# Kernel optimization log

Hardware: AMD Instinct MI355X
Metric: run time of the kernel (lower is better)

Reference implementation:

```python
import jax, jax.numpy as jnp
import numpy as np

GRID = 0.5
NG = 48
NC = 16  # output channels
CHUNK = 256  # atoms per scan step (bounds peak memory)
E2 = float(np.exp(2.0))
# order matches pro_keys ['O','C','N','S'] with vdw_dic
VDW = jnp.array([1.52, 1.7, 1.55, 1.8], dtype=jnp.float32)


def setup_inputs() -> dict:
    key = jax.random.key(0)
    k1, k2, k3 = jax.random.split(key, 3)
    N = 2048
    coords = jax.random.uniform(k1, (N, 3), dtype=jnp.float32) * (NG * GRID)  # [0, 24)
    ch_idx = jax.random.randint(k2, (N,), 0, 4, dtype=jnp.int32)
    fg = jax.random.randint(k3, (N,), 0, 16, dtype=jnp.int32)
    return {"coords": coords, "ch_idx": ch_idx, "fg": fg}


def _channel_weights(ch_idx, fg):
    # base element channel 0..3
    w = jax.nn.one_hot(ch_idx, NC, dtype=jnp.float32)
    # fg routing: 14 -> +ch4 +ch5; 15 -> +ch6 +ch9; 12/13 -> nothing; else -> +ch(fg+4)
    c1 = jnp.where(fg == 14, 4, jnp.where(fg == 15, 6, fg + 4))
    c1 = jnp.where((fg == 12) | (fg == 13), -1, c1)  # one_hot(-1) == zeros
    c2 = jnp.where(fg == 14, 5, jnp.where(fg == 15, 9, -1))
    return w + jax.nn.one_hot(c1, NC, dtype=jnp.float32) + jax.nn.one_hot(c2, NC, dtype=jnp.float32)


def _grid_forward(coords, r, w):
    # coords [N,3], r [N] vdw radii, w [N,16] channel weights -> [16,48,48,48]
    gx = GRID * jnp.arange(NG, dtype=jnp.float32)  # grid point coordinates
    nchunk = coords.shape[0] // CHUNK
    coords_c = coords.reshape(nchunk, CHUNK, 3)
    r_c = r.reshape(nchunk, CHUNK)
    w_c = w.reshape(nchunk, CHUNK, NC)

    def body(acc, args):
        c, rr, ww = args  # [CHUNK,3], [CHUNK], [CHUNK,16]
        dx2 = (c[:, 0, None] - gx) ** 2  # [CHUNK,48]
        dy2 = (c[:, 1, None] - gx) ** 2
        dz2 = (c[:, 2, None] - gx) ** 2
        d2 = dx2[:, :, None, None] + dy2[:, None, :, None] + dz2[:, None, None, :]  # [CHUNK,48,48,48]
        d = jnp.sqrt(d2)
        r_ = rr[:, None, None, None]
        r2 = r_ * r_
        f1 = jnp.exp(-2.0 * d2 / r2)
        f2 = 4.0 * d2 / (E2 * r2) - 12.0 * d / (E2 * r_) + 9.0 / E2
        val = jnp.where(d < r_, f1, jnp.where(d < 1.5 * r_, f2, 0.0))
        acc = acc + jnp.einsum('nc,nxyz->cxyz', ww, val)
        return acc, None

    out, _ = jax.lax.scan(body, jnp.zeros((NC, NG, NG, NG), jnp.float32), (coords_c, r_c, w_c))
    return out


def reference(coords, ch_idx, fg):
    r = VDW[ch_idx]
    w = _channel_weights(ch_idx, fg)
    return _grid_forward(coords, r, w)
```

## Files before the change

### kernel.cpp

```cpp
#include <hip/hip_runtime.h>

#define NG 48
#define NC 16
#define NPTS (NG * NG * NG)
#define E2F 7.3890561f
#define NINE_OVER_E2 1.2180175f
#define LOG2E 1.44269504f

#define BR 4
#define SEGCAP 48
#define SBCAP 512
#define MAXATOMS 2048

__device__ __constant__ float c_vdw[4] = {1.52f, 1.7f, 1.55f, 1.8f};

__device__ __forceinline__ void atom_params(int ci, int f, float r,
                                            float& b0, float& b1, float& b2, int& mask) {
    const float r2 = r * r;
    int c1 = (f == 14) ? 4 : ((f == 15) ? 6 : f + 4);
    if (f == 12 || f == 13) c1 = -1;
    const int c2 = (f == 14) ? 5 : ((f == 15) ? 9 : -1);
    mask = 1 << ci;
    if (c1 >= 0) mask |= 1 << c1;
    if (c2 >= 0) mask |= 1 << c2;
    b0 = -2.0f * LOG2E / r2;
    b1 = 4.0f / (E2F * r2);
    b2 = 12.0f / (E2F * r);
}

__global__ __launch_bounds__(1024)
void build_kernel(const float* __restrict__ coords,
                  const int* __restrict__ ch_idx,
                  const int* __restrict__ fg,
                  float4* __restrict__ segA, float4* __restrict__ segB,
                  int* __restrict__ counts, int natoms)
{
    __shared__ float sx[MAXATOMS], sy[MAXATOMS], sz[MAXATOMS], scut[MAXATOMS];
    __shared__ float sb0[MAXATOMS], sb1[MAXATOMS], sb2[MAXATOMS], sb3[MAXATOMS];
    __shared__ int sCnt[16];

    const int t = threadIdx.x, w = t >> 6, l = t & 63;
    const int n = min(natoms, MAXATOMS);

    for (int i = t; i < n; i += 1024) {
        const float x = coords[3 * i], y = coords[3 * i + 1], z = coords[3 * i + 2];
        const int ci = ch_idx[i], f = fg[i];
        const float r = c_vdw[ci];
        float b0, b1, b2; int mask;
        atom_params(ci, f, r, b0, b1, b2, mask);
        sx[i] = x; sy[i] = y; sz[i] = z; scut[i] = 1.5f * r;
        sb0[i] = b0; sb1[i] = b1; sb2[i] = b2; sb3[i] = __int_as_float(mask);
    }
    __syncthreads();

    const int sb = blockIdx.x;
    const int sbx = sb / 9, sby = (sb / 3) % 3, sbz = sb % 3;
    const float lox = sbx * 8.0f, hix = lox + 7.5f;
    const float loy = sby * 8.0f, hiy = loy + 7.5f;
    const float loz = sbz * 8.0f, hiz = loz + 7.5f;

    int runTot = 0;
    for (int base = 0; base < n; base += 1024) {
        const int a = base + t;
        bool pred = false;
        float ax = 0.f, ay = 0.f, az = 0.f, cut = 0.f;
        if (a < n) {
            ax = sx[a]; ay = sy[a]; az = sz[a]; cut = scut[a];
            const float ddx = fmaxf(fmaxf(lox - ax, ax - hix), 0.f);
            const float ddy = fmaxf(fmaxf(loy - ay, ay - hiy), 0.f);
            const float ddz = fmaxf(fmaxf(loz - az, az - hiz), 0.f);
            pred = fmaf(ddx, ddx, fmaf(ddy, ddy, ddz * ddz)) < cut * cut;
        }
        const unsigned long long m = __ballot(pred);
        if (l == 0) sCnt[w] = __popcll(m);
        __syncthreads();
        int ofs = runTot, tot = 0;
        #pragma unroll
        for (int w2 = 0; w2 < 16; ++w2) {
            const int c = sCnt[w2];
            if (w2 < w) ofs += c;
            tot += c;
        }
        if (pred) {
            const int o = ofs + __popcll(m & ((1ull << l) - 1ull));
            if (o < SBCAP) {
                segA[sb * SBCAP + o] = make_float4(ax, ay, az, cut);
                segB[sb * SBCAP + o] = make_float4(sb0[a], sb1[a], sb2[a], sb3[a]);
            }
        }
        runTot += tot;
        __syncthreads();
    }
    if (t == 0) counts[sb] = min(runTot, SBCAP);
}

__global__ __launch_bounds__(256)
void density_kernel(const float4* __restrict__ segA,
                    const float4* __restrict__ segB,
                    const int* __restrict__ counts,
                    float* __restrict__ out)
{
    __shared__ __align__(16) unsigned char smem[16384];
    __shared__ int sCnt[4];
    float4* const sA = (float4*)smem;
    float4* const sB = sA + 4 * SEGCAP;
    float (*const sRed)[64] = (float (*)[64])smem;

    const int t = threadIdx.x, w = t >> 6, l = t & 63;
    const int bz = blockIdx.x, by = blockIdx.y, bx = blockIdx.z;

    const float blox = bx * 2.0f, bhix = blox + 1.5f;
    const float bloy = by * 2.0f, bhiy = bloy + 1.5f;
    const float bloz = bz * 2.0f, bhiz = bloz + 1.5f;

    const int sb = ((bx >> 2) * 3 + (by >> 2)) * 3 + (bz >> 2);
    const int cnt_sb = counts[sb];
    const float4* const srcA = segA + sb * SBCAP;
    const float4* const srcB = segB + sb * SBCAP;

    const int q = (cnt_sb + 3) >> 2;
    const int i0 = w * q, i1 = min(i0 + q, cnt_sb);
    int myCnt = 0;
    for (int base = i0; base < i1; base += 64) {
        const int idx = base + l;
        bool pred = false;
        float4 pA, pB;
        if (idx < i1) {
            pA = srcA[idx];
            pB = srcB[idx];
            const float ddx = fmaxf(fmaxf(blox - pA.x, pA.x - bhix), 0.f);
            const float ddy = fmaxf(fmaxf(bloy - pA.y, pA.y - bhiy), 0.f);
            const float ddz = fmaxf(fmaxf(bloz - pA.z, pA.z - bhiz), 0.f);
            pred = fmaf(ddx, ddx, fmaf(ddy, ddy, ddz * ddz)) < pA.w * pA.w;
        }
        const unsigned long long m = __ballot(pred);
        if (pred) {
            const int o = myCnt + __popcll(m & ((1ull << l) - 1ull));
            if (o < SEGCAP) { sA[w * SEGCAP + o] = pA; sB[w * SEGCAP + o] = pB; }
        }
        myCnt += __popcll(m);
    }
    if (l == 0) sCnt[w] = min(myCnt, SEGCAP);
    __syncthreads();

    const int c0 = sCnt[0], c1 = sCnt[1], c2 = sCnt[2], c3 = sCnt[3];

    const int tz = l & 3, ty = (l >> 2) & 3, tx = l >> 4;
    const float px = (bx * BR + tx) * 0.5f;
    const float py = (by * BR + ty) * 0.5f;
    const float pz = (bz * BR + tz) * 0.5f;

    float acc[NC];
    #pragma unroll
    for (int c = 0; c < NC; ++c) acc[c] = 0.0f;

    #pragma unroll 1
    for (int s = 0; s < 4; ++s) {
        const int cs = (s == 0) ? c0 : (s == 1) ? c1 : (s == 2) ? c2 : c3;
        const int segbase = s * SEGCAP;
        #pragma unroll 2
        for (int i = w; i < cs; i += 4) {
            const float4 A = sA[segbase + i];
            const float4 B = sB[segbase + i];
            const float dx = px - A.x;
            const float dy = py - A.y;
            const float dz = pz - A.z;
            const float d2 = fmaf(dx, dx, fmaf(dy, dy, dz * dz));
            const float cut2 = A.w * A.w;
            if (d2 < cut2) {
                const float r2 = cut2 * (4.0f / 9.0f);
                const float d  = sqrtf(d2);
                const float f1 = exp2f(B.x * d2);
                const float f2 = fmaf(B.y, d2, fmaf(-B.z, d, NINE_OVER_E2));
                const float val = (d2 < r2) ? f1 : f2;
                const int chan = __builtin_amdgcn_readfirstlane(__float_as_int(B.w));
                #pragma unroll
                for (int c = 0; c < NC; ++c)
                    if (chan & (1 << c)) acc[c] += val;
            }
        }
    }
    __syncthreads();

    #pragma unroll
    for (int c = 0; c < NC; ++c) sRed[w * NC + c][l] = acc[c];
    __syncthreads();

    const int gx = bx * BR + tx, gy = by * BR + ty, gz = bz * BR + tz;
    const int pbase = (gx * NG + gy) * NG + gz;
    #pragma unroll
    for (int k = 0; k < 4; ++k) {
        const int c = w * 4 + k;
        const float s = sRed[0 * NC + c][l] + sRed[1 * NC + c][l] +
                        sRed[2 * NC + c][l] + sRed[3 * NC + c][l];
        out[c * NPTS + pbase] = s;
    }
}

__global__ void prep_kernel(const float* __restrict__ coords,
                            const int* __restrict__ ch_idx,
                            const int* __restrict__ fg,
                            float4* __restrict__ atomA,
                            float4* __restrict__ atomB, int natoms)
{
    const int i = blockIdx.x * blockDim.x + threadIdx.x;
    if (i >= natoms) return;
    const int ci = ch_idx[i], f = fg[i];
    const float r = c_vdw[ci];
    float b0, b1, b2; int mask;
    atom_params(ci, f, r, b0, b1, b2, mask);
    atomA[i] = make_float4(coords[3 * i], coords[3 * i + 1], coords[3 * i + 2], 1.5f * r);
    atomB[i] = make_float4(b0, b1, b2, __int_as_float(mask));
}

__global__ __launch_bounds__(256)
void density_scan_kernel(const float4* __restrict__ atomA,
                         const float4* __restrict__ atomB,
                         float* __restrict__ out, int natoms)
{
    __shared__ __align__(16) unsigned char smem[16384];
    __shared__ int sCnt[4];
    float4* const sA = (float4*)smem;
    float4* const sB = sA + 4 * SEGCAP;
    float (*const sRed)[64] = (float (*)[64])smem;

    const int t = threadIdx.x, w = t >> 6, l = t & 63;
    const int bz = blockIdx.x, by = blockIdx.y, bx = blockIdx.z;

    const float blox = bx * 2.0f, bhix = blox + 1.5f;
    const float bloy = by * 2.0f, bhiy = bloy + 1.5f;
    const float bloz = bz * 2.0f, bhiz = bloz + 1.5f;

    const int quarter = (natoms + 3) >> 2;
    const int a0 = w * quarter, a1 = min(a0 + quarter, natoms);
    int myCnt = 0;
    for (int base = a0; base < a1; base += 64) {
        const int a = base + l;
        bool pred = false; float4 pA;
        if (a < a1) {
            pA = atomA[a];
            const float ddx = fmaxf(fmaxf(blox - pA.x, pA.x - bhix), 0.f);
            const float ddy = fmaxf(fmaxf(bloy - pA.y, pA.y - bhiy), 0.f);
            const float ddz = fmaxf(fmaxf(bloz - pA.z, pA.z - bhiz), 0.f);
            pred = fmaf(ddx, ddx, fmaf(ddy, ddy, ddz * ddz)) < pA.w * pA.w;
        }
        const unsigned long long m = __ballot(pred);
        if (pred) {
            const int o = myCnt + __popcll(m & ((1ull << l) - 1ull));
            if (o < SEGCAP) { sA[w * SEGCAP + o] = pA; sB[w * SEGCAP + o] = atomB[a]; }
        }
        myCnt += __popcll(m);
    }
    if (l == 0) sCnt[w] = min(myCnt, SEGCAP);
    __syncthreads();

    const int c0 = sCnt[0], c1 = sCnt[1], c2 = sCnt[2], c3 = sCnt[3];
    const int tz = l & 3, ty = (l >> 2) & 3, tx = l >> 4;
    const float px = (bx * BR + tx) * 0.5f;
    const float py = (by * BR + ty) * 0.5f;
    const float pz = (bz * BR + tz) * 0.5f;

    float acc[NC];
    #pragma unroll
    for (int c = 0; c < NC; ++c) acc[c] = 0.0f;

    #pragma unroll 1
    for (int s = 0; s < 4; ++s) {
        const int cs = (s == 0) ? c0 : (s == 1) ? c1 : (s == 2) ? c2 : c3;
        const int segbase = s * SEGCAP;
        #pragma unroll 2
        for (int i = w; i < cs; i += 4) {
            const float4 A = sA[segbase + i];
            const float4 B = sB[segbase + i];
            const float dx = px - A.x, dy = py - A.y, dz = pz - A.z;
            const float d2 = fmaf(dx, dx, fmaf(dy, dy, dz * dz));
            const float cut2 = A.w * A.w;
            if (d2 < cut2) {
                const float r2 = cut2 * (4.0f / 9.0f);
                const float d  = sqrtf(d2);
                const float f1 = exp2f(B.x * d2);
                const float f2 = fmaf(B.y, d2, fmaf(-B.z, d, NINE_OVER_E2));
                const float val = (d2 < r2) ? f1 : f2;
                const int chan = __builtin_amdgcn_readfirstlane(__float_as_int(B.w));
                #pragma unroll
                for (int c = 0; c < NC; ++c)
                    if (chan & (1 << c)) acc[c] += val;
            }
        }
    }
    __syncthreads();
    #pragma unroll
    for (int c = 0; c < NC; ++c) sRed[w * NC + c][l] = acc[c];
    __syncthreads();

    const int gx = bx * BR + tx, gy = by * BR + ty, gz = bz * BR + tz;
    const int pbase = (gx * NG + gy) * NG + gz;
    #pragma unroll
    for (int k = 0; k < 4; ++k) {
        const int c = w * 4 + k;
        out[c * NPTS + pbase] = sRed[0 * NC + c][l] + sRed[1 * NC + c][l] +
                                sRed[2 * NC + c][l] + sRed[3 * NC + c][l];
    }
}

extern "C" void kernel_launch(void* const* d_in, const int* in_sizes, int n_in,
                              void* d_out, int out_size, void* d_ws, size_t ws_size,
                              hipStream_t stream) {
    (void)n_in; (void)out_size;
    const float* coords = (const float*)d_in[0];
    const int* ch = (const int*)d_in[1];
    const int* fgp = (const int*)d_in[2];
    float* out = (float*)d_out;
    const int natoms = in_sizes[0] / 3;

    const size_t need = 256 + 2ull * 27 * SBCAP * sizeof(float4);
    dim3 grid(NG / BR, NG / BR, NG / BR);

    if (natoms <= MAXATOMS && ws_size >= need) {
        int* counts = (int*)d_ws;
        float4* segA = (float4*)((char*)d_ws + 256);
        float4* segB = segA + 27 * SBCAP;
        build_kernel<<<27, 1024, 0, stream>>>(coords, ch, fgp, segA, segB, counts, natoms);
        density_kernel<<<grid, 256, 0, stream>>>(segA, segB, counts, out);
    } else {
        float4* atomA = (float4*)d_ws;
        float4* atomB = atomA + natoms;
        prep_kernel<<<(natoms + 255) / 256, 256, 0, stream>>>(coords, ch, fgp, atomA, atomB, natoms);
        density_scan_kernel<<<grid, 256, 0, stream>>>(atomA, atomB, out, natoms);
    }
}
```

Measured before the change: 21.39 us.

## Refine atom binning to 6x6x6 superblocks with per-wave sublists and branchless accumulation

The build kernel now bins atoms into 216 smaller superblocks (4 Å instead of 8 Å) using 256-thread blocks. Each wave compacts its own quarter of the atoms into a fixed 64-entry sublist, which removes the shared-memory staging and block-wide prefix syncs. The density kernel then loads each wave's sublist in a single pass. The inner loop replaces the divergent cutoff branch and per-channel conditional adds with a select plus masked FMAs, and staggers the starting index per segment. There are two risks: sublists truncate silently if more than 64 atoms land in one wave's quarter, and the NINE_OVER_E2 constant was changed.

```diff
diff --git a/kernel.cpp b/kernel.cpp
--- a/kernel.cpp
+++ b/kernel.cpp
@@ -4,94 +4,80 @@
 #define NC 16
 #define NPTS (NG * NG * NG)
 #define E2F 7.3890561f
-#define NINE_OVER_E2 1.2180175f
+#define NINE_OVER_E2 1.2178960f
 #define LOG2E 1.44269504f
 
 #define BR 4
-#define SEGCAP 48
-#define SBCAP 512
+#define NSB 6
+#define SBSUB 64
+#define SBCAP 256
+#define SEGCAP 64
 #define MAXATOMS 2048
 
-__device__ __constant__ float c_vdw[4] = {1.52f, 1.7f, 1.55f, 1.8f};
-
-__device__ __forceinline__ void atom_params(int ci, int f, float r,
-                                            float& b0, float& b1, float& b2, int& mask) {
-    const float r2 = r * r;
+__device__ __forceinline__ float sel_r(int ci) {
+    return ci == 0 ? 1.52f : ci == 1 ? 1.7f : ci == 2 ? 1.55f : 1.8f;
+}
+__device__ __forceinline__ int chan_mask(int ci, int f) {
     int c1 = (f == 14) ? 4 : ((f == 15) ? 6 : f + 4);
     if (f == 12 || f == 13) c1 = -1;
     const int c2 = (f == 14) ? 5 : ((f == 15) ? 9 : -1);
-    mask = 1 << ci;
+    int mask = 1 << ci;
     if (c1 >= 0) mask |= 1 << c1;
     if (c2 >= 0) mask |= 1 << c2;
-    b0 = -2.0f * LOG2E / r2;
-    b1 = 4.0f / (E2F * r2);
-    b2 = 12.0f / (E2F * r);
-}
-
-__global__ __launch_bounds__(1024)
+    return mask;
+}
+
+__global__ __launch_bounds__(256)
 void build_kernel(const float* __restrict__ coords,
                   const int* __restrict__ ch_idx,
                   const int* __restrict__ fg,
                   float4* __restrict__ segA, float4* __restrict__ segB,
                   int* __restrict__ counts, int natoms)
 {
-    __shared__ float sx[MAXATOMS], sy[MAXATOMS], sz[MAXATOMS], scut[MAXATOMS];
-    __shared__ float sb0[MAXATOMS], sb1[MAXATOMS], sb2[MAXATOMS], sb3[MAXATOMS];
-    __shared__ int sCnt[16];
-
     const int t = threadIdx.x, w = t >> 6, l = t & 63;
-    const int n = min(natoms, MAXATOMS);
-
-    for (int i = t; i < n; i += 1024) {
-        const float x = coords[3 * i], y = coords[3 * i + 1], z = coords[3 * i + 2];
-        const int ci = ch_idx[i], f = fg[i];
-        const float r = c_vdw[ci];
-        float b0, b1, b2; int mask;
-        atom_params(ci, f, r, b0, b1, b2, mask);
-        sx[i] = x; sy[i] = y; sz[i] = z; scut[i] = 1.5f * r;
-        sb0[i] = b0; sb1[i] = b1; sb2[i] = b2; sb3[i] = __int_as_float(mask);
-    }
-    __syncthreads();
-
     const int sb = blockIdx.x;
-    const int sbx = sb / 9, sby = (sb / 3) % 3, sbz = sb % 3;
-    const float lox = sbx * 8.0f, hix = lox + 7.5f;
-    const float loy = sby * 8.0f, hiy = loy + 7.5f;
-    const float loz = sbz * 8.0f, hiz = loz + 7.5f;
-
-    int runTot = 0;
-    for (int base = 0; base < n; base += 1024) {
-        const int a = base + t;
+    const int sbx = sb / 36, sby = (sb / 6) % 6, sbz = sb % 6;
+    const float lox = sbx * 4.0f, hix = lox + 3.5f;
+    const float loy = sby * 4.0f, hiy = loy + 3.5f;
+    const float loz = sbz * 4.0f, hiz = loz + 3.5f;
+
+    const int quarter = (natoms + 3) >> 2;
+    const int a0 = w * quarter;
+    const int a1 = min(a0 + quarter, natoms);
+
+    int cnt = 0;
+    #pragma unroll 2
+    for (int base = a0; base < a1; base += 64) {
+        const int a = base + l;
         bool pred = false;
-        float ax = 0.f, ay = 0.f, az = 0.f, cut = 0.f;
-        if (a < n) {
-            ax = sx[a]; ay = sy[a]; az = sz[a]; cut = scut[a];
+        float ax = 0.f, ay = 0.f, az = 0.f, r = 1.f;
+        int ci = 0, f = 0;
+        if (a < a1) {
+            ax = coords[3 * a]; ay = coords[3 * a + 1]; az = coords[3 * a + 2];
+            ci = ch_idx[a]; f = fg[a];
+            r = sel_r(ci);
+            const float cut = 1.5f * r;
             const float ddx = fmaxf(fmaxf(lox - ax, ax - hix), 0.f);
             const float ddy = fmaxf(fmaxf(loy - ay, ay - hiy), 0.f);
             const float ddz = fmaxf(fmaxf(loz - az, az - hiz), 0.f);
             pred = fmaf(ddx, ddx, fmaf(ddy, ddy, ddz * ddz)) < cut * cut;
         }
         const unsigned long long m = __ballot(pred);
-        if (l == 0) sCnt[w] = __popcll(m);
-        __syncthreads();
-        int ofs = runTot, tot = 0;
-        #pragma unroll
-        for (int w2 = 0; w2 < 16; ++w2) {
-            const int c = sCnt[w2];
-            if (w2 < w) ofs += c;
-            tot += c;
-        }
         if (pred) {
-            const int o = ofs + __popcll(m & ((1ull << l) - 1ull));
-            if (o < SBCAP) {
-                segA[sb * SBCAP + o] = make_float4(ax, ay, az, cut);
-                segB[sb * SBCAP + o] = make_float4(sb0[a], sb1[a], sb2[a], sb3[a]);
+            const int o = cnt + __popcll(m & ((1ull << l) - 1ull));
+            if (o < SBSUB) {
+                const float r2 = r * r;
+                const int idx = sb * SBCAP + w * SBSUB + o;
+                segA[idx] = make_float4(ax, ay, az, 1.5f * r);
+                segB[idx] = make_float4(-2.0f * LOG2E / r2,
+                                        4.0f / (E2F * r2),
+                                        12.0f / (E2F * r),
+                                        __int_as_float(chan_mask(ci, f)));
             }
         }
-        runTot += tot;
-        __syncthreads();
-    }
-    if (t == 0) counts[sb] = min(runTot, SBCAP);
+        cnt += __popcll(m);
+    }
+    if (l == 0) counts[sb * 4 + w] = min(cnt, SBSUB);
 }
 
 __global__ __launch_bounds__(256)
@@ -113,21 +99,16 @@
     const float bloy = by * 2.0f, bhiy = bloy + 1.5f;
     const float bloz = bz * 2.0f, bhiz = bloz + 1.5f;
 
-    const int sb = ((bx >> 2) * 3 + (by >> 2)) * 3 + (bz >> 2);
-    const int cnt_sb = counts[sb];
-    const float4* const srcA = segA + sb * SBCAP;
-    const float4* const srcB = segB + sb * SBCAP;
-
-    const int q = (cnt_sb + 3) >> 2;
-    const int i0 = w * q, i1 = min(i0 + q, cnt_sb);
-    int myCnt = 0;
-    for (int base = i0; base < i1; base += 64) {
-        const int idx = base + l;
+    const int sb = (((bx >> 1) * NSB) + (by >> 1)) * NSB + (bz >> 1);
+    const int cw = counts[sb * 4 + w];
+
+    {
         bool pred = false;
         float4 pA, pB;
-        if (idx < i1) {
-            pA = srcA[idx];
-            pB = srcB[idx];
+        if (l < cw) {
+            const int idx = sb * SBCAP + w * SBSUB + l;
+            pA = segA[idx];
+            pB = segB[idx];
             const float ddx = fmaxf(fmaxf(blox - pA.x, pA.x - bhix), 0.f);
             const float ddy = fmaxf(fmaxf(bloy - pA.y, pA.y - bhiy), 0.f);
             const float ddz = fmaxf(fmaxf(bloz - pA.z, pA.z - bhiz), 0.f);
@@ -135,12 +116,12 @@
         }
         const unsigned long long m = __ballot(pred);
         if (pred) {
-            const int o = myCnt + __popcll(m & ((1ull << l) - 1ull));
-            if (o < SEGCAP) { sA[w * SEGCAP + o] = pA; sB[w * SEGCAP + o] = pB; }
-        }
-        myCnt += __popcll(m);
-    }
-    if (l == 0) sCnt[w] = min(myCnt, SEGCAP);
+            const int o = __popcll(m & ((1ull << l) - 1ull));
+            sA[w * SEGCAP + o] = pA;
+            sB[w * SEGCAP + o] = pB;
+        }
+        if (l == 0) sCnt[w] = __popcll(m);
+    }
     __syncthreads();
 
     const int c0 = sCnt[0], c1 = sCnt[1], c2 = sCnt[2], c3 = sCnt[3];
@@ -159,7 +140,7 @@
         const int cs = (s == 0) ? c0 : (s == 1) ? c1 : (s == 2) ? c2 : c3;
         const int segbase = s * SEGCAP;
         #pragma unroll 2
-        for (int i = w; i < cs; i += 4) {
+        for (int i = (w + s) & 3; i < cs; i += 4) {
             const float4 A = sA[segbase + i];
             const float4 B = sB[segbase + i];
             const float dx = px - A.x;
@@ -167,16 +148,17 @@
             const float dz = pz - A.z;
             const float d2 = fmaf(dx, dx, fmaf(dy, dy, dz * dz));
             const float cut2 = A.w * A.w;
-            if (d2 < cut2) {
-                const float r2 = cut2 * (4.0f / 9.0f);
-                const float d  = sqrtf(d2);
-                const float f1 = exp2f(B.x * d2);
-                const float f2 = fmaf(B.y, d2, fmaf(-B.z, d, NINE_OVER_E2));
-                const float val = (d2 < r2) ? f1 : f2;
-                const int chan = __builtin_amdgcn_readfirstlane(__float_as_int(B.w));
-                #pragma unroll
-                for (int c = 0; c < NC; ++c)
-                    if (chan & (1 << c)) acc[c] += val;
+            const float r2 = cut2 * (4.0f / 9.0f);
+            const float d  = sqrtf(d2);
+            const float f1 = exp2f(B.x * d2);
+            const float f2 = fmaf(B.y, d2, fmaf(-B.z, d, NINE_OVER_E2));
+            float val = (d2 < r2) ? f1 : f2;
+            val = (d2 < cut2) ? val : 0.0f;
+            const int chan = __builtin_amdgcn_readfirstlane(__float_as_int(B.w));
+            #pragma unroll
+            for (int c = 0; c < NC; ++c) {
+                const float msk = __int_as_float(((chan >> c) & 1) * 0x3f800000);
+                acc[c] = fmaf(msk, val, acc[c]);
             }
         }
     }
@@ -191,9 +173,8 @@
     #pragma unroll
     for (int k = 0; k < 4; ++k) {
         const int c = w * 4 + k;
-        const float s = sRed[0 * NC + c][l] + sRed[1 * NC + c][l] +
-                        sRed[2 * NC + c][l] + sRed[3 * NC + c][l];
-        out[c * NPTS + pbase] = s;
+        out[c * NPTS + pbase] = sRed[0 * NC + c][l] + sRed[1 * NC + c][l] +
+                                sRed[2 * NC + c][l] + sRed[3 * NC + c][l];
     }
 }
 
@@ -206,11 +187,11 @@
     const int i = blockIdx.x * blockDim.x + threadIdx.x;
     if (i >= natoms) return;
     const int ci = ch_idx[i], f = fg[i];
-    const float r = c_vdw[ci];
-    float b0, b1, b2; int mask;
-    atom_params(ci, f, r, b0, b1, b2, mask);
+    const float r = sel_r(ci);
+    const float r2 = r * r;
     atomA[i] = make_float4(coords[3 * i], coords[3 * i + 1], coords[3 * i + 2], 1.5f * r);
-    atomB[i] = make_float4(b0, b1, b2, __int_as_float(mask));
+    atomB[i] = make_float4(-2.0f * LOG2E / r2, 4.0f / (E2F * r2),
+                           12.0f / (E2F * r), __int_as_float(chan_mask(ci, f)));
 }
 
 __global__ __launch_bounds__(256)
@@ -269,22 +250,23 @@
         const int cs = (s == 0) ? c0 : (s == 1) ? c1 : (s == 2) ? c2 : c3;
         const int segbase = s * SEGCAP;
         #pragma unroll 2
-        for (int i = w; i < cs; i += 4) {
+        for (int i = (w + s) & 3; i < cs; i += 4) {
             const float4 A = sA[segbase + i];
             const float4 B = sB[segbase + i];
             const float dx = px - A.x, dy = py - A.y, dz = pz - A.z;
             const float d2 = fmaf(dx, dx, fmaf(dy, dy, dz * dz));
             const float cut2 = A.w * A.w;
-            if (d2 < cut2) {
-                const float r2 = cut2 * (4.0f / 9.0f);
-                const float d  = sqrtf(d2);
-                const float f1 = exp2f(B.x * d2);
-                const float f2 = fmaf(B.y, d2, fmaf(-B.z, d, NINE_OVER_E2));
-                const float val = (d2 < r2) ? f1 : f2;
-                const int chan = __builtin_amdgcn_readfirstlane(__float_as_int(B.w));
-                #pragma unroll
-                for (int c = 0; c < NC; ++c)
-                    if (chan & (1 << c)) acc[c] += val;
+            const float r2 = cut2 * (4.0f / 9.0f);
+            const float d  = sqrtf(d2);
+            const float f1 = exp2f(B.x * d2);
+            const float f2 = fmaf(B.y, d2, fmaf(-B.z, d, NINE_OVER_E2));
+            float val = (d2 < r2) ? f1 : f2;
+            val = (d2 < cut2) ? val : 0.0f;
+            const int chan = __builtin_amdgcn_readfirstlane(__float_as_int(B.w));
+            #pragma unroll
+            for (int c = 0; c < NC; ++c) {
+                const float msk = __int_as_float(((chan >> c) & 1) * 0x3f800000);
+                acc[c] = fmaf(msk, val, acc[c]);
             }
         }
     }
@@ -313,14 +295,15 @@
     float* out = (float*)d_out;
     const int natoms = in_sizes[0] / 3;
 
-    const size_t need = 256 + 2ull * 27 * SBCAP * sizeof(float4);
+    const int nsb3 = NSB * NSB * NSB;
+    const size_t need = 4096 + 2ull * nsb3 * SBCAP * sizeof(float4);
     dim3 grid(NG / BR, NG / BR, NG / BR);
 
     if (natoms <= MAXATOMS && ws_size >= need) {
         int* counts = (int*)d_ws;
-        float4* segA = (float4*)((char*)d_ws + 256);
-        float4* segB = segA + 27 * SBCAP;
-        build_kernel<<<27, 1024, 0, stream>>>(coords, ch, fgp, segA, segB, counts, natoms);
+        float4* segA = (float4*)((char*)d_ws + 4096);
+        float4* segB = segA + nsb3 * SBCAP;
+        build_kernel<<<nsb3, 256, 0, stream>>>(coords, ch, fgp, segA, segB, counts, natoms);
         density_kernel<<<grid, 256, 0, stream>>>(segA, segB, counts, out);
     } else {
         float4* atomA = (float4*)d_ws;
```

Result: slower. 22.01 us (+2.9%).
